# Performance work log

Hardware: AMD Instinct MI355X
Metric: run time of the kernel (lower is better)

Reference implementation:

```python
import jax, jax.numpy as jnp
import numpy as np

DELTA = 5.0          # weight on positive BCE term
R = 0.01             # hard-negative fraction
M, N = 4096, 16384   # batch rows, memory-bank size
NUM_HARD = int(R * (N - 1))  # int(r * neg_count); each row has exactly 1 positive


def setup_inputs() -> dict:
    key = jax.random.key(0)
    k1, k2 = jax.random.split(key)
    inputs = jax.random.normal(k1, (M, N), dtype=jnp.float32)
    targets = jax.random.randint(k2, (M,), 0, N)
    return {"inputs": inputs, "targets": targets}


def reference(inputs, targets):
    m, n = inputs.shape
    rows = jnp.arange(m)
    # positive logit per row (one-hot scatter => exactly one positive)
    pos = inputs[rows, targets]                          # [m]
    # BCE with logits, target=1: softplus(-x); mean over the single positive
    l_pos = jax.nn.softplus(-pos)                        # [m]
    # exclude positive from negatives by sinking it to -inf, then hard top-k
    neg_inf = jnp.finfo(inputs.dtype).min
    masked = inputs.at[rows, targets].set(neg_inf)       # [m, n]
    hard_neg, _ = jax.lax.top_k(masked, NUM_HARD)        # [m, NUM_HARD]
    # BCE with logits, target=0: softplus(x); mean over hard negatives
    l_neg = jnp.mean(jax.nn.softplus(hard_neg), axis=1)  # [m]
    return jnp.mean(DELTA * l_pos + l_neg)
```

## Files before the change

kernel.cpp:

```cpp
#include <hip/hip_runtime.h>
#include <stdint.h>

#define M_ROWS 4096
#define N_COLS 16384
#define K_HARD 163
#define DELTA_W 5.0f
#define BLOCK  256
#define SLOTS  12
#define CAP    1024
#define NB     1024
#define SMALL  64
#define THRESH 2.0f
#define KEY_MIN 0xC0000000u

__device__ __forceinline__ uint32_t f2key(float x) {
    uint32_t u = __float_as_uint(x);
    return u ^ (uint32_t)(((int32_t)u >> 31) | 0x80000000u);
}
__device__ __forceinline__ float key2f(uint32_t k) {
    uint32_t u = (k & 0x80000000u) ? (k & 0x7fffffffu) : ~k;
    return __uint_as_float(u);
}
__device__ __forceinline__ float softplus_f(float x) {
    return fmaxf(x, 0.0f) + log1pf(__expf(-fabsf(x)));
}

__device__ void pivot_scan(const uint32_t* hist, int K,
                           int* part, int* pivot, int* krem) {
    const int t = threadIdx.x;
    const int bpt = NB / BLOCK;
    const int base = t * bpt;
    int mypart = 0;
    for (int i = 0; i < bpt; ++i) mypart += (int)hist[base + i];
    part[t] = mypart;
    __syncthreads();
    for (int off = 1; off < BLOCK; off <<= 1) {
        int v = part[t];
        if (t + off < BLOCK) v += part[t + off];
        __syncthreads();
        part[t] = v;
        __syncthreads();
    }
    const int above = part[t] - mypart;
    if (above < K && above + mypart >= K) {
        int running = above;
        for (int b = base + bpt - 1; b >= base; --b) {
            int c = (int)hist[b];
            if (running < K && running + c >= K) { *pivot = b; *krem = K - running; }
            running += c;
        }
    }
    __syncthreads();
}

__global__ __launch_bounds__(BLOCK) void mmcl_kernel(
        const float* __restrict__ inputs,
        const int* __restrict__ targets,
        float* __restrict__ out) {
    __shared__ float    s_slots_f[BLOCK * SLOTS];
    __shared__ uint32_t s_cand[CAP];
    __shared__ int s_wt[4], s_wm[4];
    __shared__ int s_found, s_pivot, s_krem, s_nsmall;
    __shared__ uint32_t s_skey[SMALL];
    __shared__ int s_sidx[SMALL];
    __shared__ float s_fw[4];

    const int row = blockIdx.x;
    const int t = threadIdx.x;
    const int lane = t & 63;
    const int wid = t >> 6;
    const float* rowp = inputs + (size_t)row * N_COLS;
    const int target = targets[row];

    if (t == 0) s_found = -1;

    float* myslots = s_slots_f + t * SLOTS;
    uint32_t cnt = 0;
    const float4* rp4 = (const float4*)rowp;
#pragma unroll 4
    for (int it = 0; it < N_COLS / (BLOCK * 4); ++it) {
        const float4 v = rp4[it * BLOCK + t];
        myslots[min(cnt, (uint32_t)(SLOTS - 1))] = v.x; cnt += (v.x >= THRESH);
        myslots[min(cnt, (uint32_t)(SLOTS - 1))] = v.y; cnt += (v.y >= THRESH);
        myslots[min(cnt, (uint32_t)(SLOTS - 1))] = v.z; cnt += (v.z >= THRESH);
        myslots[min(cnt, (uint32_t)(SLOTS - 1))] = v.w; cnt += (v.w >= THRESH);
    }

    const int stored = (int)min(cnt, (uint32_t)SLOTS);
    int inc = stored;
    for (int off = 1; off < 64; off <<= 1) {
        int y = __shfl_up(inc, off);
        if (lane >= off) inc += y;
    }
    int mx = (int)cnt;
    for (int off = 1; off < 64; off <<= 1)
        mx = max(mx, __shfl_xor(mx, off));
    if (lane == 63) { s_wt[wid] = inc; }
    if (lane == 0)  { s_wm[wid] = mx; }
    __syncthreads();
    const int w0 = s_wt[0], w1 = s_wt[1], w2 = s_wt[2], w3 = s_wt[3];
    const int total = w0 + w1 + w2 + w3;
    const int maxc = max(max(s_wm[0], s_wm[1]), max(s_wm[2], s_wm[3]));
    const int wbase = (wid > 0 ? w0 : 0) + (wid > 1 ? w1 : 0) + (wid > 2 ? w2 : 0);
    const int myoff = wbase + inc - stored;
    for (int c = 0; c < stored; ++c) {
        const int d = myoff + c;
        if (d < CAP) s_cand[d] = f2key(myslots[c]);
    }
    __syncthreads();

    const float pos = rowp[target];
    const uint32_t tkey = f2key(pos);
    const int tclamp = min(total, CAP);
    if (pos >= THRESH) {
        for (int i = t; i < tclamp; i += BLOCK)
            if (s_cand[i] == tkey) { atomicCAS(&s_found, -1, i); break; }
    }
    __syncthreads();
    int ncand = total;
    if (s_found >= 0) {
        ncand = total - 1;
        if (t == 0) s_cand[s_found] = s_cand[ncand];
    }
    __syncthreads();

    const bool fast = (maxc <= SLOTS) && (total <= CAP) && (ncand >= K_HARD);
    bool needfb = !fast;
    float local = 0.0f;

    uint32_t* hist = (uint32_t*)s_slots_f;

    if (fast) {
        for (int i = t; i < NB; i += BLOCK) hist[i] = 0;
        __syncthreads();
        for (int i = t; i < ncand; i += BLOCK)
            atomicAdd(&hist[min((s_cand[i] - KEY_MIN) >> 14, (uint32_t)(NB - 1))], 1u);
        __syncthreads();

        const int base4 = t * 4;
        const int c0 = (int)hist[base4], c1 = (int)hist[base4 + 1],
                  c2 = (int)hist[base4 + 2], c3 = (int)hist[base4 + 3];
        const int own = c0 + c1 + c2 + c3;
        int suf = own;
        for (int off = 1; off < 64; off <<= 1) {
            int y = __shfl_down(suf, off);
            if (lane + off < 64) suf += y;
        }
        if (lane == 0) s_wt[wid] = suf;
        if (t == 0) s_nsmall = 0;
        __syncthreads();
        int wsuf = 0;
        for (int w = wid + 1; w < 4; ++w) wsuf += s_wt[w];
        int run = wsuf + (suf - own);
        {
            const int cs[4] = {c0, c1, c2, c3};
            for (int b = 3; b >= 0; --b) {
                const int c = cs[b];
                if (run < K_HARD && run + c >= K_HARD) {
                    s_pivot = base4 + b; s_krem = K_HARD - run;
                }
                run += c;
            }
        }
        __syncthreads();
        const uint32_t B = (uint32_t)s_pivot;
        const int krem = s_krem;

        for (int i = t; i < ncand; i += BLOCK) {
            const uint32_t k = s_cand[i];
            const uint32_t kb = min((k - KEY_MIN) >> 14, (uint32_t)(NB - 1));
            if (kb > B) local += softplus_f(key2f(k));
            else if (kb == B) {
                const int d = atomicAdd(&s_nsmall, 1);
                if (d < SMALL) { s_skey[d] = k; s_sidx[d] = i; }
            }
        }
        __syncthreads();
        const int m = s_nsmall;
        if (m > SMALL) { needfb = true; local = 0.0f; }
        else {
            for (int i = t; i < m; i += BLOCK) {
                const uint32_t ki = s_skey[i]; const int ii = s_sidx[i];
                int r = 0;
                for (int j = 0; j < m; ++j) {
                    const uint32_t kj = s_skey[j];
                    r += (kj > ki) || (kj == ki && s_sidx[j] < ii);
                }
                if (r < krem) local += softplus_f(key2f(ki));
            }
        }
    }

    if (needfb) {
        local = 0.0f;
        int* part = (int*)s_cand;
        for (int i = t; i < NB; i += BLOCK) hist[i] = 0;
        __syncthreads();
        for (int j = t; j < N_COLS; j += BLOCK) {
            if (j == target) continue;
            atomicAdd(&hist[f2key(rowp[j]) >> 22], 1u);
        }
        __syncthreads();
        pivot_scan(hist, K_HARD, part, &s_pivot, &s_krem);
        const int p1 = s_pivot, k1r = s_krem;

        for (int i = t; i < NB; i += BLOCK) hist[i] = 0;
        __syncthreads();
        for (int j = t; j < N_COLS; j += BLOCK) {
            if (j == target) continue;
            const uint32_t k = f2key(rowp[j]);
            if ((int)(k >> 22) == p1) atomicAdd(&hist[(k >> 12) & 1023u], 1u);
        }
        __syncthreads();
        pivot_scan(hist, k1r, part, &s_pivot, &s_krem);
        const uint32_t pref2 = ((uint32_t)p1 << 10) | (uint32_t)s_pivot;
        const int k2r = s_krem;

        for (int i = t; i < NB; i += BLOCK) hist[i] = 0;
        __syncthreads();
        for (int j = t; j < N_COLS; j += BLOCK) {
            if (j == target) continue;
            const uint32_t k = f2key(rowp[j]);
            if ((k >> 12) == pref2) atomicAdd(&hist[(k >> 2) & 1023u], 1u);
        }
        __syncthreads();
        pivot_scan(hist, k2r, part, &s_pivot, &s_krem);
        const uint32_t pref3 = (pref2 << 10) | (uint32_t)s_pivot;
        const int k3r = s_krem;

        for (int i = t; i < 4; i += BLOCK) hist[i] = 0;
        __syncthreads();
        for (int j = t; j < N_COLS; j += BLOCK) {
            if (j == target) continue;
            const uint32_t k = f2key(rowp[j]);
            if ((k >> 2) == pref3) atomicAdd(&hist[k & 3u], 1u);
        }
        __syncthreads();
        if (t == 0) {
            int running = 0;
            for (int b = 3; b >= 0; --b) {
                const int c = (int)hist[b];
                if (running < k3r && running + c >= k3r) {
                    s_pivot = b; s_krem = k3r - running;
                }
                running += c;
            }
        }
        __syncthreads();
        const uint32_t T = (pref3 << 2) | (uint32_t)s_pivot;
        const int tie = s_krem;

        for (int j = t; j < N_COLS; j += BLOCK) {
            if (j == target) continue;
            const uint32_t k = f2key(rowp[j]);
            if (k > T) local += softplus_f(key2f(k));
        }
        if (t == 0) local += (float)tie * softplus_f(key2f(T));
    }

    for (int off = 32; off > 0; off >>= 1) local += __shfl_down(local, off);
    if (lane == 0) s_fw[wid] = local;
    __syncthreads();
    if (t == 0) {
        const float tot = s_fw[0] + s_fw[1] + s_fw[2] + s_fw[3];
        const float l_neg = tot / (float)K_HARD;
        const float l_pos = softplus_f(-pos);
        const float rowval = (DELTA_W * l_pos + l_neg) * (1.0f / (float)M_ROWS);
        atomicAdd(out, rowval);
    }
}

__global__ void mmcl_zero_out(float* out) { out[0] = 0.0f; }

extern "C" void kernel_launch(void* const* d_in, const int* in_sizes, int n_in,
                              void* d_out, int out_size, void* d_ws, size_t ws_size,
                              hipStream_t stream) {
    const float* inputs = (const float*)d_in[0];
    const int* targets = (const int*)d_in[1];
    float* out = (float*)d_out;
    mmcl_zero_out<<<1, 1, 0, stream>>>(out);
    mmcl_kernel<<<M_ROWS, BLOCK, 0, stream>>>(inputs, targets, out);
}
```

Baseline: 360.4 us.

## Replace per-thread slot buffers with shared atomic candidate append and fused histogram

Drops the per-thread 12-slot shared scratch and the wave prefix-scan compaction. Threshold-passing values are now appended to the shared candidate list through an atomic counter, and the coarse histogram is built in the same pass, so the separate compaction and histogram passes go away. Shared memory use shrinks a lot and launch bounds request 4 blocks per CU, aiming at higher occupancy. The cost is contended shared atomics and a nondeterministic candidate order; the fix-up that removes the positive now also decrements its histogram bin.

```diff
diff --git a/kernel.cpp b/kernel.cpp
--- a/kernel.cpp
+++ b/kernel.cpp
@@ -6,7 +6,6 @@
 #define K_HARD 163
 #define DELTA_W 5.0f
 #define BLOCK  256
-#define SLOTS  12
 #define CAP    1024
 #define NB     1024
 #define SMALL  64
@@ -53,14 +52,54 @@
     __syncthreads();
 }
 
-__global__ __launch_bounds__(BLOCK) void mmcl_kernel(
+#define PROCESS4(v)                                                            \
+    do {                                                                       \
+        const bool b0 = ((v).x >= THRESH);                                     \
+        const bool b1 = ((v).y >= THRESH);                                     \
+        const bool b2 = ((v).z >= THRESH);                                     \
+        const bool b3 = ((v).w >= THRESH);                                     \
+        const int kk = (int)b0 + (int)b1 + (int)b2 + (int)b3;                  \
+        if (kk) {                                                              \
+            int d = atomicAdd(&s_cnt, kk);                                     \
+            if (b0) {                                                          \
+                const uint32_t key = f2key((v).x);                             \
+                if (d < CAP) s_cand[d] = key;                                  \
+                atomicAdd(&s_hist[min((key - KEY_MIN) >> 14,                   \
+                                      (uint32_t)(NB - 1))], 1u);               \
+                ++d;                                                           \
+            }                                                                  \
+            if (b1) {                                                          \
+                const uint32_t key = f2key((v).y);                             \
+                if (d < CAP) s_cand[d] = key;                                  \
+                atomicAdd(&s_hist[min((key - KEY_MIN) >> 14,                   \
+                                      (uint32_t)(NB - 1))], 1u);               \
+                ++d;                                                           \
+            }                                                                  \
+            if (b2) {                                                          \
+                const uint32_t key = f2key((v).z);                             \
+                if (d < CAP) s_cand[d] = key;                                  \
+                atomicAdd(&s_hist[min((key - KEY_MIN) >> 14,                   \
+                                      (uint32_t)(NB - 1))], 1u);               \
+                ++d;                                                           \
+            }                                                                  \
+            if (b3) {                                                          \
+                const uint32_t key = f2key((v).w);                             \
+                if (d < CAP) s_cand[d] = key;                                  \
+                atomicAdd(&s_hist[min((key - KEY_MIN) >> 14,                   \
+                                      (uint32_t)(NB - 1))], 1u);               \
+                ++d;                                                           \
+            }                                                                  \
+        }                                                                      \
+    } while (0)
+
+__global__ __launch_bounds__(BLOCK, 4) void mmcl_kernel(
         const float* __restrict__ inputs,
         const int* __restrict__ targets,
         float* __restrict__ out) {
-    __shared__ float    s_slots_f[BLOCK * SLOTS];
     __shared__ uint32_t s_cand[CAP];
-    __shared__ int s_wt[4], s_wm[4];
-    __shared__ int s_found, s_pivot, s_krem, s_nsmall;
+    __shared__ uint32_t s_hist[NB];
+    __shared__ int s_wt[4];
+    __shared__ int s_cnt, s_found, s_pivot, s_krem, s_nsmall;
     __shared__ uint32_t s_skey[SMALL];
     __shared__ int s_sidx[SMALL];
     __shared__ float s_fw[4];
@@ -71,45 +110,26 @@
     const int wid = t >> 6;
     const float* rowp = inputs + (size_t)row * N_COLS;
     const int target = targets[row];
-
-    if (t == 0) s_found = -1;
-
-    float* myslots = s_slots_f + t * SLOTS;
-    uint32_t cnt = 0;
+    const float pos = rowp[target];
+
+    for (int i = t; i < NB; i += BLOCK) s_hist[i] = 0;
+    if (t == 0) { s_cnt = 0; s_found = -1; s_nsmall = 0; }
+    __syncthreads();
+
     const float4* rp4 = (const float4*)rowp;
-#pragma unroll 4
-    for (int it = 0; it < N_COLS / (BLOCK * 4); ++it) {
-        const float4 v = rp4[it * BLOCK + t];
-        myslots[min(cnt, (uint32_t)(SLOTS - 1))] = v.x; cnt += (v.x >= THRESH);
-        myslots[min(cnt, (uint32_t)(SLOTS - 1))] = v.y; cnt += (v.y >= THRESH);
-        myslots[min(cnt, (uint32_t)(SLOTS - 1))] = v.z; cnt += (v.z >= THRESH);
-        myslots[min(cnt, (uint32_t)(SLOTS - 1))] = v.w; cnt += (v.w >= THRESH);
-    }
-
-    const int stored = (int)min(cnt, (uint32_t)SLOTS);
-    int inc = stored;
-    for (int off = 1; off < 64; off <<= 1) {
-        int y = __shfl_up(inc, off);
-        if (lane >= off) inc += y;
-    }
-    int mx = (int)cnt;
-    for (int off = 1; off < 64; off <<= 1)
-        mx = max(mx, __shfl_xor(mx, off));
-    if (lane == 63) { s_wt[wid] = inc; }
-    if (lane == 0)  { s_wm[wid] = mx; }
-    __syncthreads();
-    const int w0 = s_wt[0], w1 = s_wt[1], w2 = s_wt[2], w3 = s_wt[3];
-    const int total = w0 + w1 + w2 + w3;
-    const int maxc = max(max(s_wm[0], s_wm[1]), max(s_wm[2], s_wm[3]));
-    const int wbase = (wid > 0 ? w0 : 0) + (wid > 1 ? w1 : 0) + (wid > 2 ? w2 : 0);
-    const int myoff = wbase + inc - stored;
-    for (int c = 0; c < stored; ++c) {
-        const int d = myoff + c;
-        if (d < CAP) s_cand[d] = f2key(myslots[c]);
-    }
-    __syncthreads();
-
-    const float pos = rowp[target];
+    for (int g = 0; g < N_COLS / (BLOCK * 16); ++g) {
+        const float4 v0 = rp4[(g * 4 + 0) * BLOCK + t];
+        const float4 v1 = rp4[(g * 4 + 1) * BLOCK + t];
+        const float4 v2 = rp4[(g * 4 + 2) * BLOCK + t];
+        const float4 v3 = rp4[(g * 4 + 3) * BLOCK + t];
+        PROCESS4(v0);
+        PROCESS4(v1);
+        PROCESS4(v2);
+        PROCESS4(v3);
+    }
+    __syncthreads();
+    const int total = s_cnt;
+
     const uint32_t tkey = f2key(pos);
     const int tclamp = min(total, CAP);
     if (pos >= THRESH) {
@@ -120,26 +140,21 @@
     int ncand = total;
     if (s_found >= 0) {
         ncand = total - 1;
-        if (t == 0) s_cand[s_found] = s_cand[ncand];
-    }
-    __syncthreads();
-
-    const bool fast = (maxc <= SLOTS) && (total <= CAP) && (ncand >= K_HARD);
+        if (t == 0) {
+            if (ncand < CAP) s_cand[s_found] = s_cand[ncand];
+            s_hist[min((tkey - KEY_MIN) >> 14, (uint32_t)(NB - 1))] -= 1u;
+        }
+    }
+    __syncthreads();
+
+    const bool fast = (total <= CAP) && (ncand >= K_HARD);
     bool needfb = !fast;
     float local = 0.0f;
 
-    uint32_t* hist = (uint32_t*)s_slots_f;
-
     if (fast) {
-        for (int i = t; i < NB; i += BLOCK) hist[i] = 0;
-        __syncthreads();
-        for (int i = t; i < ncand; i += BLOCK)
-            atomicAdd(&hist[min((s_cand[i] - KEY_MIN) >> 14, (uint32_t)(NB - 1))], 1u);
-        __syncthreads();
-
         const int base4 = t * 4;
-        const int c0 = (int)hist[base4], c1 = (int)hist[base4 + 1],
-                  c2 = (int)hist[base4 + 2], c3 = (int)hist[base4 + 3];
+        const int c0 = (int)s_hist[base4], c1 = (int)s_hist[base4 + 1],
+                  c2 = (int)s_hist[base4 + 2], c3 = (int)s_hist[base4 + 3];
         const int own = c0 + c1 + c2 + c3;
         int suf = own;
         for (int off = 1; off < 64; off <<= 1) {
@@ -147,7 +162,6 @@
             if (lane + off < 64) suf += y;
         }
         if (lane == 0) s_wt[wid] = suf;
-        if (t == 0) s_nsmall = 0;
         __syncthreads();
         int wsuf = 0;
         for (int w = wid + 1; w < 4; ++w) wsuf += s_wt[w];
@@ -194,6 +208,7 @@
     if (needfb) {
         local = 0.0f;
         int* part = (int*)s_cand;
+        uint32_t* hist = s_hist;
         for (int i = t; i < NB; i += BLOCK) hist[i] = 0;
         __syncthreads();
         for (int j = t; j < N_COLS; j += BLOCK) {
```

Measured after the change: 372.2 us. 3.3% more time.
